# Kernel tuning notes

Hardware: AMD Instinct MI355X
Metric: run time of the kernel (lower is better)

## Reference

```python
import jax, jax.numpy as jnp
import numpy as np

N_NODES = 50000
N_EDGES = 800000
NODE_DIM = 128
HIDDEN = 256
LATENT = 128
COND = 5


def setup_inputs() -> dict:
    key = jax.random.key(0)
    ks = jax.random.split(key, 10)
    s = lambda d: 1.0 / np.sqrt(d)
    return {
        "node_features": jax.random.normal(ks[0], (N_NODES, NODE_DIM), jnp.float32),
        "conditions": jax.random.normal(ks[1], (COND,), jnp.float32),
        "src": jax.random.randint(ks[2], (N_EDGES,), 0, N_NODES, jnp.int32),
        "dst": jax.random.randint(ks[3], (N_EDGES,), 0, N_NODES, jnp.int32),
        "W1": jax.random.normal(ks[4], (NODE_DIM, HIDDEN), jnp.float32) * s(NODE_DIM),
        "b1": jnp.zeros((HIDDEN,), jnp.float32),
        "W2": jax.random.normal(ks[5], (HIDDEN, HIDDEN), jnp.float32) * s(HIDDEN),
        "b2": jnp.zeros((HIDDEN,), jnp.float32),
        "Wfc": jax.random.normal(ks[6], (HIDDEN + COND, LATENT), jnp.float32) * s(HIDDEN + COND),
        "bfc": jnp.zeros((LATENT,), jnp.float32),
        "Wmean": jax.random.normal(ks[7], (LATENT, LATENT), jnp.float32) * s(LATENT),
        "bmean": jnp.zeros((LATENT,), jnp.float32),
        "Wlogvar": jax.random.normal(ks[8], (LATENT, LATENT), jnp.float32) * s(LATENT),
        "blogvar": jnp.zeros((LATENT,), jnp.float32),
    }


def _graph_conv(x, src, dst, W, b, n_nodes):
    # gather source-node features along edges, sum-aggregate onto targets,
    # then linear transform: standard GraphConv (sum aggregation)
    agg = jax.ops.segment_sum(x[src], dst, num_segments=n_nodes)  # [N, d]
    return agg @ W + b


def reference(node_features, conditions, src, dst,
              W1, b1, W2, b2, Wfc, bfc, Wmean, bmean, Wlogvar, blogvar):
    n = node_features.shape[0]
    x = jax.nn.relu(_graph_conv(node_features, src, dst, W1, b1, n))  # [N, H]
    x = jax.nn.relu(_graph_conv(x, src, dst, W2, b2, n))              # [N, H]
    pooled = jnp.mean(x, axis=0)                                      # [H]
    h = jax.nn.relu(jnp.concatenate([pooled, conditions], axis=-1) @ Wfc + bfc)
    z_mean = h @ Wmean + bmean
    z_logvar = h @ Wlogvar + blogvar
    return z_mean, z_logvar
```

## Files before the change

kernel.cpp:

```cpp
#include <hip/hip_runtime.h>

#define N_NODES   50000
#define N_EDGES   800000
#define NODE_DIM  128
#define HIDDEN    256
#define LATENT    128
#define COND      5

#define NB        196
#define P1_CHUNK  4096
#define P1_GRID   ((N_EDGES + P1_CHUNK - 1) / P1_CHUNK)

typedef unsigned int uint;
typedef unsigned short ushort;
typedef unsigned char uchar;

typedef __attribute__((ext_vector_type(8))) short bf16x8;
typedef __attribute__((ext_vector_type(4))) float f32x4;

static __device__ __forceinline__ ushort f32_to_bf16(float f) {
    union { float f; uint u; } v; v.f = f;
    uint r = v.u + 0x7FFF + ((v.u >> 16) & 1);
    return (ushort)(r >> 16);
}
static __device__ __forceinline__ uint pack_bf16(float lo, float hi) {
    return (uint)f32_to_bf16(lo) | ((uint)f32_to_bf16(hi) << 16);
}

static __device__ __forceinline__ void gload_lds16(const void* g, void* l) {
    __builtin_amdgcn_global_load_lds(
        (const __attribute__((address_space(1))) unsigned int*)(unsigned long long)(uintptr_t)g,
        (__attribute__((address_space(3))) unsigned int*)(unsigned int)(uintptr_t)l,
        16, 0, 0);
}


#if __has_builtin(__builtin_amdgcn_cvt_pk_f32_fp8) && __has_builtin(__builtin_amdgcn_cvt_pk_fp8_f32)
#define HW_FP8 1
#endif

#ifndef HW_FP8
static __device__ __forceinline__ float dec1_fp8(uint b) {
    uint sgn = b & 0x80, mag = b & 0x7f;
    float v;
    if (mag >= 8) {
        union { uint u; float f; } t;
        t.u = (((mag >> 3) + 120) << 23) | ((mag & 7) << 20);
        v = t.f;
    } else {
        v = (float)mag * 0.001953125f;
    }
    return sgn ? -v : v;
}
static __device__ __forceinline__ uchar enc1_fp8(float f) {
    float a = fabsf(f);
    uint s = (f < 0.f) ? 0x80u : 0u;
    if (!(a >= 0.015625f)) {
        int q = (int)(a * 512.f + 0.5f);
        if (q > 7) q = 7;
        return (uchar)(s | (uint)q);
    }
    if (a >= 448.f) return (uchar)(s | 0x7E);
    union { float f; uint u; } t; t.f = a;
    uint e = (t.u >> 23) - 120;
    uint m = (t.u >> 20) & 7;
    uint rem = t.u & 0xFFFFF;
    uint v = (e << 3) | m;
    if (rem > 0x80000 || (rem == 0x80000 && (v & 1))) v++;
    if (v > 0x7E) v = 0x7E;
    return (uchar)(s | v);
}
#endif

static __device__ __forceinline__ void dec4_add(uint u, float* acc) {
#ifdef HW_FP8
    auto lo = __builtin_amdgcn_cvt_pk_f32_fp8((int)u, false);
    auto hi = __builtin_amdgcn_cvt_pk_f32_fp8((int)u, true);
    acc[0] += lo[0]; acc[1] += lo[1]; acc[2] += hi[0]; acc[3] += hi[1];
#else
    acc[0] += dec1_fp8(u & 0xff);
    acc[1] += dec1_fp8((u >> 8) & 0xff);
    acc[2] += dec1_fp8((u >> 16) & 0xff);
    acc[3] += dec1_fp8(u >> 24);
#endif
}
static __device__ __forceinline__ void dec2_add(uint u, float* acc) {
#ifdef HW_FP8
    auto lo = __builtin_amdgcn_cvt_pk_f32_fp8((int)u, false);
    acc[0] += lo[0]; acc[1] += lo[1];
#else
    acc[0] += dec1_fp8(u & 0xff);
    acc[1] += dec1_fp8((u >> 8) & 0xff);
#endif
}
static __device__ __forceinline__ uint enc2_fp8(float a, float b) {
#ifdef HW_FP8
    return (uint)__builtin_amdgcn_cvt_pk_fp8_f32(a, b, 0, false) & 0xFFFFu;
#else
    return (uint)enc1_fp8(a) | ((uint)enc1_fp8(b) << 8);
#endif
}
static __device__ __forceinline__ uchar enc1(float v) {
#ifdef HW_FP8
    return (uchar)(__builtin_amdgcn_cvt_pk_fp8_f32(v, v, 0, false) & 0xff);
#else
    return enc1_fp8(v);
#endif
}


#define NF4   (N_NODES * NODE_DIM / 4)
#define PREP1 (NF4 + NODE_DIM * HIDDEN)
#define PREP2 (PREP1 + HIDDEN * HIDDEN)
#define PREP3 (PREP2 + HIDDEN)
#define PREP4 (PREP3 + NB)
#define PREP5 (PREP4 + NB)
#define PREP6 (PREP5 + 1)

__global__ void prep_kernel(const float* __restrict__ nf,
                            const float* __restrict__ W1, const float* __restrict__ W2,
                            uchar* __restrict__ nf_fp8,
                            ushort* __restrict__ Wst1, ushort* __restrict__ Wst2,
                            float* __restrict__ pooled,
                            int* __restrict__ bcount, int* __restrict__ bcursor2,
                            int* __restrict__ hcnt) {
    int id = blockIdx.x * blockDim.x + threadIdx.x;
    if (id < NF4) {
        float4 v = reinterpret_cast<const float4*>(nf)[id];
        uint w = enc2_fp8(v.x, v.y) | (enc2_fp8(v.z, v.w) << 16);
        reinterpret_cast<uint*>(nf_fp8)[id] = w;
    } else if (id < PREP1) {
        int i = id - NF4;
        int k = i >> 8, c = i & 255;
        int idx = ((((k >> 5) * 16) + (((k & 31) >> 3) * 4 + (c >> 6))) * 64 + (c & 63)) * 8 + (k & 7);
        Wst1[idx] = f32_to_bf16(W1[i]);
    } else if (id < PREP2) {
        int i = id - PREP1;
        int k = i >> 8, c = i & 255;
        int idx = ((((k >> 5) * 16) + (((k & 31) >> 3) * 4 + (c >> 6))) * 64 + (c & 63)) * 8 + (k & 7);
        Wst2[idx] = f32_to_bf16(W2[i]);
    } else if (id < PREP3) {
        pooled[id - PREP2] = 0.f;
    } else if (id < PREP4) {
        bcount[id - PREP3] = 0;
    } else if (id < PREP5) {
        bcursor2[id - PREP4] = 0;
    } else if (id < PREP6) {
        hcnt[0] = 0;
    }
}


__global__ __launch_bounds__(256) void bcount_kernel(const int* __restrict__ dst,
                                                     int* __restrict__ bcount) {
    __shared__ int cnt[NB];
    const int t = threadIdx.x;
    for (int i = t; i < NB; i += 256) cnt[i] = 0;
    __syncthreads();
    const int base = blockIdx.x * P1_CHUNK;
#pragma unroll
    for (int i = 0; i < 16; ++i) {
        int e = base + i * 256 + t;
        if (e < N_EDGES) atomicAdd(&cnt[dst[e] >> 8], 1);
    }
    __syncthreads();
    for (int i = t; i < NB; i += 256)
        if (cnt[i] > 0) atomicAdd(&bcount[i], cnt[i]);
}

__global__ __launch_bounds__(256) void bwrite_kernel(const int* __restrict__ src,
                                                     const int* __restrict__ dst,
                                                     const int* __restrict__ bcount,
                                                     int* __restrict__ bcursor2,
                                                     uint* __restrict__ pair_buf) {
    __shared__ int s[256];
    __shared__ int cnt[NB];
    __shared__ int gbase[NB];
    const int t = threadIdx.x;
    s[t] = (t < NB) ? bcount[t] : 0;
    __syncthreads();
    for (int off = 1; off < 256; off <<= 1) {
        int v = (t >= off) ? s[t - off] : 0;
        __syncthreads();
        s[t] += v;
        __syncthreads();
    }
    for (int i = t; i < NB; i += 256) cnt[i] = 0;
    __syncthreads();

    const int base = blockIdx.x * P1_CHUNK;
    uint pk[16];
    int  bk[16], lr[16];
    bool ok[16];
#pragma unroll
    for (int i = 0; i < 16; ++i) {
        int e = base + i * 256 + t;
        ok[i] = e < N_EDGES;
        if (ok[i]) {
            int sv = src[e], d = dst[e];
            pk[i] = (uint)sv | ((uint)d << 16);
            bk[i] = d >> 8;
        }
    }
#pragma unroll
    for (int i = 0; i < 16; ++i)
        if (ok[i]) lr[i] = atomicAdd(&cnt[bk[i]], 1);
    __syncthreads();
    if (t < NB) {
        int c = cnt[t];
        if (c > 0) gbase[t] = ((t > 0) ? s[t - 1] : 0) + atomicAdd(&bcursor2[t], c);
    }
    __syncthreads();
#pragma unroll
    for (int i = 0; i < 16; ++i)
        if (ok[i]) pair_buf[gbase[bk[i]] + lr[i]] = pk[i];
}

__global__ __launch_bounds__(256) void csrloc_kernel(const uint* __restrict__ pair_buf,
                                                     const int* __restrict__ bcount,
                                                     int* __restrict__ offsets,
                                                     ushort* __restrict__ csr) {
    __shared__ int s[256];
    __shared__ int lcnt[256];
    __shared__ int loff[256];
    __shared__ int lcur[256];
    const int t = threadIdx.x;
    const int b = blockIdx.x;
    s[t] = (t < NB) ? bcount[t] : 0;
    __syncthreads();
    for (int off = 1; off < 256; off <<= 1) {
        int v = (t >= off) ? s[t - off] : 0;
        __syncthreads();
        s[t] += v;
        __syncthreads();
    }
    const int e0 = (b > 0) ? s[b - 1] : 0;
    const int e1 = s[b];
    lcnt[t] = 0;
    lcur[t] = 0;
    __syncthreads();

    for (int j = e0 + t; j < e1; j += 256)
        atomicAdd(&lcnt[(pair_buf[j] >> 16) & 255], 1);
    __syncthreads();

    const int myc = lcnt[t];
    s[t] = myc;
    __syncthreads();
    for (int off = 1; off < 256; off <<= 1) {
        int v = (t >= off) ? s[t - off] : 0;
        __syncthreads();
        s[t] += v;
        __syncthreads();
    }
    const int lofft = s[t] - myc;
    loff[t] = lofft;
    const int node = (b << 8) + t;
    if (node < N_NODES) offsets[node] = e0 + lofft;
    if (b == 0 && t == 0) offsets[N_NODES] = N_EDGES;
    __syncthreads();

    for (int j = e0 + t; j < e1; j += 256) {
        uint p = pair_buf[j];
        int dl = (int)(p >> 16) & 255;
        int r = atomicAdd(&lcur[dl], 1);
        csr[e0 + loff[dl] + r] = (ushort)(p & 0xFFFFu);
    }
}


template <int D>
__global__ __launch_bounds__(256) void agg_kernel(const uchar* __restrict__ x,
                                                  const int* __restrict__ offsets,
                                                  const ushort* __restrict__ csr,
                                                  ushort* __restrict__ out) {
    constexpr int BPL = D / 64;
    int node = (blockIdx.x * blockDim.x + threadIdx.x) >> 6;
    int lane = threadIdx.x & 63;
    if (node >= N_NODES) return;
    int j0 = __builtin_amdgcn_readfirstlane(offsets[node]);
    int j1 = __builtin_amdgcn_readfirstlane(offsets[node + 1]);

    float acc[BPL];
#pragma unroll
    for (int i = 0; i < BPL; ++i) acc[i] = 0.f;

    const uchar* base = x + lane * BPL;
    const int il = lane & 15;

    int idxv = (j0 + il < j1) ? (int)csr[j0 + il] : 0;

    for (int jb = j0; jb < j1; jb += 16) {
        int idxn = (jb + 16 + il < j1) ? (int)csr[jb + 16 + il] : 0;
        int n = j1 - jb; n = (n > 16) ? 16 : n;
        uint u[16];
        if (n == 16) {
#pragma unroll
            for (int i = 0; i < 16; ++i) {
                int s = __shfl(idxv, i);
                if constexpr (BPL == 4)
                    u[i] = *reinterpret_cast<const uint*>(base + (size_t)s * D);
                else
                    u[i] = *reinterpret_cast<const ushort*>(base + (size_t)s * D);
            }
#pragma unroll
            for (int i = 0; i < 16; ++i) {
                if constexpr (BPL == 4) dec4_add(u[i], acc); else dec2_add(u[i], acc);
            }
        } else {
#pragma unroll
            for (int i = 0; i < 16; ++i) {
                if (i < n) {
                    int s = __shfl(idxv, i);
                    if constexpr (BPL == 4)
                        u[i] = *reinterpret_cast<const uint*>(base + (size_t)s * D);
                    else
                        u[i] = *reinterpret_cast<const ushort*>(base + (size_t)s * D);
                }
            }
#pragma unroll
            for (int i = 0; i < 16; ++i) {
                if (i < n) {
                    if constexpr (BPL == 4) dec4_add(u[i], acc); else dec2_add(u[i], acc);
                }
            }
        }
        idxv = idxn;
    }

    if constexpr (BPL == 4) {
        uint2 o;
        o.x = pack_bf16(acc[0], acc[1]);
        o.y = pack_bf16(acc[2], acc[3]);
        *reinterpret_cast<uint2*>(out + (size_t)node * D + lane * 4) = o;
    } else {
        *reinterpret_cast<uint*>(out + (size_t)node * D + lane * 2) = pack_bf16(acc[0], acc[1]);
    }
}


__global__ __launch_bounds__(256) void gemm1_kernel(const ushort* __restrict__ A,
                                                    const ushort* __restrict__ Wst,
                                                    const float* __restrict__ bias,
                                                    uchar* __restrict__ Xout, int nblk) {
    constexpr int K = NODE_DIM;
    constexpr int NSTEP = K / 32;
    constexpr int WB    = NSTEP * 8 * 1024;
    constexpr int AB    = NSTEP * 4 * 1024;
    constexpr int NT    = (N_NODES + 63) / 64;
    __shared__ uchar lds[WB + 2 * AB];

    const int t    = threadIdx.x;
    const int lane = t & 63;
    const int wv   = t >> 6;
    const int fr   = lane & 15;
    const int kgl  = lane >> 4;
    const int colhalf = blockIdx.x & 1;
    const int stride  = nblk >> 1;

    const int kx = (lane & 3) ^ ((lane >> 3) & 3);

#pragma unroll
    for (int j = 0; j < NSTEP * 2; ++j) {
        const int lc = wv * (NSTEP * 2) + j;
        const int ks = lc >> 3, r = lc & 7;
        const int kg = r >> 1, ccl = r & 1;
        gload_lds16(Wst + ((size_t)ks * 16 + kg * 4 + colhalf * 2 + ccl) * 512 + lane * 8,
                    &lds[lc * 1024]);
    }

    auto stageA = [&](int buf, int row0) {
#pragma unroll
        for (int j = 0; j < NSTEP; ++j) {
            const int c  = wv * NSTEP + j;
            const int ks = c >> 2, rt = c & 3;
            gload_lds16(A + (size_t)(row0 + rt * 16 + (lane >> 2)) * K + ks * 32 + kx * 8,
                        &lds[WB + buf * AB + c * 1024]);
        }
    };

    const int rowsel = (wv & 1) * 2;
    const int colsel = wv >> 1;
    const int col0   = colhalf * 128 + colsel * 64;
    float bcol[4];
#pragma unroll
    for (int ct = 0; ct < 4; ++ct) bcol[ct] = bias[col0 + ct * 16 + fr];
    const int mrow = kgl * 4;
    const int aswz = (kgl ^ ((fr >> 1) & 3)) * 16;

    int tile = blockIdx.x >> 1;
    stageA(0, tile * 64);
    __syncthreads();

    for (int buf = 0; tile < NT; tile += stride, buf ^= 1) {
        const int tn = tile + stride;
        if (tn < NT) stageA(buf ^ 1, tn * 64);

        f32x4 acc[2][4];
#pragma unroll
        for (int rt = 0; rt < 2; ++rt)
#pragma unroll
            for (int ct = 0; ct < 4; ++ct)
                acc[rt][ct] = (f32x4){0.f, 0.f, 0.f, 0.f};

        const uchar* ab = &lds[WB + buf * AB];
#pragma unroll
        for (int ks = 0; ks < NSTEP; ++ks) {
            bf16x8 af[2], bfv[4];
#pragma unroll
            for (int rt = 0; rt < 2; ++rt)
                af[rt] = *reinterpret_cast<const bf16x8*>(ab + (ks * 4 + rowsel + rt) * 1024 + fr * 64 + aswz);
#pragma unroll
            for (int ct = 0; ct < 4; ++ct)
                bfv[ct] = *reinterpret_cast<const bf16x8*>(&lds[(ks * 8 + kgl * 2 + colsel) * 1024 + (ct * 16 + fr) * 16]);
#pragma unroll
            for (int rt = 0; rt < 2; ++rt)
#pragma unroll
                for (int ct = 0; ct < 4; ++ct)
                    acc[rt][ct] = __builtin_amdgcn_mfma_f32_16x16x32_bf16(af[rt], bfv[ct], acc[rt][ct], 0, 0, 0);
        }

        const int rowbase = tile * 64 + (wv & 1) * 32;
#pragma unroll
        for (int rt = 0; rt < 2; ++rt) {
#pragma unroll
            for (int e = 0; e < 4; ++e) {
                int m = rowbase + rt * 16 + mrow + e;
                if (m < N_NODES) {
#pragma unroll
                    for (int ct = 0; ct < 4; ++ct) {
                        float v = fmaxf(acc[rt][ct][e] + bcol[ct], 0.f);
                        Xout[(size_t)m * HIDDEN + col0 + ct * 16 + fr] = enc1(v);
                    }
                }
            }
        }
        __syncthreads();
    }
}


__global__ __launch_bounds__(256) void gemm2_kernel(const ushort* __restrict__ A,
                                                    const ushort* __restrict__ Wst,
                                                    const float* __restrict__ bias,
                                                    float* __restrict__ pooled, int nblk,
                                                    const float* __restrict__ cond,
                                                    const float* __restrict__ Wfc,
                                                    const float* __restrict__ bfc,
                                                    const float* __restrict__ Wmean,
                                                    const float* __restrict__ bmean,
                                                    const float* __restrict__ Wlogvar,
                                                    const float* __restrict__ blogvar,
                                                    float* __restrict__ outv,
                                                    int* __restrict__ hcnt) {
    constexpr int K   = HIDDEN;
    constexpr int WB  = 32768;
    constexpr int AB  = 16384;
    constexpr int NT  = (N_NODES + 31) / 32;
    __shared__ uchar lds[WB + 2 * AB];
    __shared__ int lastflag;

    const int t    = threadIdx.x;
    const int lane = t & 63;
    const int wv   = t >> 6;
    const int fr   = lane & 15;
    const int kgl  = lane >> 4;
    const int colq    = blockIdx.x & 3;
    const int stride  = nblk >> 2;

    const int kx = (lane & 3) ^ ((lane >> 3) & 3);

#pragma unroll
    for (int j = 0; j < 8; ++j) {
        const int lc = wv * 8 + j;
        const int ks = lc >> 2, kg = lc & 3;
        gload_lds16(Wst + ((size_t)ks * 16 + kg * 4 + colq) * 512 + lane * 8,
                    &lds[lc * 1024]);
    }

    auto stageA = [&](int buf, int row0) {
#pragma unroll
        for (int j = 0; j < 4; ++j) {
            const int c  = wv * 4 + j;
            const int ks = c >> 1, rh = c & 1;
            gload_lds16(A + (size_t)(row0 + rh * 16 + (lane >> 2)) * K + ks * 32 + kx * 8,
                        &lds[WB + buf * AB + c * 1024]);
        }
    };

    const int rowhalf = wv & 1;
    const int colh32  = wv >> 1;
    const int col0    = colq * 64 + colh32 * 32;
    float bcol[2];
#pragma unroll
    for (int ct = 0; ct < 2; ++ct) bcol[ct] = bias[col0 + ct * 16 + fr];
    const int mrow = kgl * 4;
    const int aswz = (kgl ^ ((fr >> 1) & 3)) * 16;

    float cs[2] = {0.f, 0.f};
    int tile = blockIdx.x >> 2;
    stageA(0, tile * 32);
    __syncthreads();

    for (int buf = 0; tile < NT; tile += stride, buf ^= 1) {
        const int tn = tile + stride;
        if (tn < NT) stageA(buf ^ 1, tn * 32);

        f32x4 acc[2];
        acc[0] = (f32x4){0.f, 0.f, 0.f, 0.f};
        acc[1] = (f32x4){0.f, 0.f, 0.f, 0.f};

        const uchar* ab = &lds[WB + buf * AB];
#pragma unroll
        for (int ks = 0; ks < 8; ++ks) {
            bf16x8 af, bfv[2];
            af = *reinterpret_cast<const bf16x8*>(ab + (ks * 2 + rowhalf) * 1024 + fr * 64 + aswz);
#pragma unroll
            for (int ct = 0; ct < 2; ++ct)
                bfv[ct] = *reinterpret_cast<const bf16x8*>(
                    &lds[(ks * 4 + kgl) * 1024 + (colh32 * 32 + ct * 16 + fr) * 16]);
#pragma unroll
            for (int ct = 0; ct < 2; ++ct)
                acc[ct] = __builtin_amdgcn_mfma_f32_16x16x32_bf16(af, bfv[ct], acc[ct], 0, 0, 0);
        }

        const int rowbase = tile * 32 + rowhalf * 16;
#pragma unroll
        for (int e = 0; e < 4; ++e) {
            int m = rowbase + mrow + e;
            if (m < N_NODES) {
                cs[0] += fmaxf(acc[0][e] + bcol[0], 0.f);
                cs[1] += fmaxf(acc[1][e] + bcol[1], 0.f);
            }
        }
        __syncthreads();
    }

#pragma unroll
    for (int ct = 0; ct < 2; ++ct) {
        cs[ct] += __shfl_xor(cs[ct], 16);
        cs[ct] += __shfl_xor(cs[ct], 32);
    }
    if (lane < 16) {
#pragma unroll
        for (int ct = 0; ct < 2; ++ct)
            atomicAdd(&pooled[col0 + ct * 16 + lane], cs[ct]);
    }

    asm volatile("s_waitcnt vmcnt(0)" ::: "memory");
    __syncthreads();
    if (t == 0) lastflag = (atomicAdd(hcnt, 1) == nblk - 1) ? 1 : 0;
    __syncthreads();
    if (lastflag) {
        float* hv = (float*)lds;
        float* hh = (float*)(lds + 2048);
        if (t < HIDDEN) hv[t] = atomicAdd(&pooled[t], 0.0f) * (1.0f / N_NODES);
        if (t < COND) hv[HIDDEN + t] = cond[t];
        __syncthreads();
        if (t < LATENT) {
            float s = bfc[t];
            for (int k = 0; k < HIDDEN + COND; ++k) s += hv[k] * Wfc[k * LATENT + t];
            hh[t] = fmaxf(s, 0.f);
        }
        __syncthreads();
        if (t < LATENT) {
            float s = bmean[t];
            for (int k = 0; k < LATENT; ++k) s += hh[k] * Wmean[k * LATENT + t];
            outv[t] = s;
        } else if (t < 2 * LATENT) {
            int j = t - LATENT;
            float s = blogvar[j];
            for (int k = 0; k < LATENT; ++k) s += hh[k] * Wlogvar[k * LATENT + j];
            outv[LATENT + j] = s;
        }
    }
}


extern "C" void kernel_launch(void* const* d_in, const int* in_sizes, int n_in,
                              void* d_out, int out_size, void* d_ws, size_t ws_size,
                              hipStream_t stream) {
    const float* node_features = (const float*)d_in[0];
    const float* conditions    = (const float*)d_in[1];
    const int*   src           = (const int*)d_in[2];
    const int*   dst           = (const int*)d_in[3];
    const float* W1  = (const float*)d_in[4];
    const float* b1  = (const float*)d_in[5];
    const float* W2  = (const float*)d_in[6];
    const float* b2  = (const float*)d_in[7];
    const float* Wfc = (const float*)d_in[8];
    const float* bfc = (const float*)d_in[9];
    const float* Wmean   = (const float*)d_in[10];
    const float* bmean   = (const float*)d_in[11];
    const float* Wlogvar = (const float*)d_in[12];
    const float* blogvar = (const float*)d_in[13];
    float* out = (float*)d_out;

    size_t o = 0;
    auto alloc = [&](size_t bytes) {
        void* p = (char*)d_ws + o;
        o += (bytes + 255) & ~(size_t)255;
        return p;
    };
    int* offsets   = (int*)alloc((size_t)(N_NODES + 1) * 4);
    int* bcount    = (int*)alloc((size_t)NB * 4);
    int* bcursor2  = (int*)alloc((size_t)NB * 4);
    int* hcnt      = (int*)alloc(4);
    uint* pair_buf = (uint*)alloc((size_t)N_EDGES * 4);
    ushort* csr    = (ushort*)alloc((size_t)N_EDGES * 2);
    float* pooled  = (float*)alloc(HIDDEN * 4);
    ushort* Wst1   = (ushort*)alloc((size_t)HIDDEN * NODE_DIM * 2);
    ushort* Wst2   = (ushort*)alloc((size_t)HIDDEN * HIDDEN * 2);
    uchar* nf_fp8  = (uchar*)alloc((size_t)N_NODES * NODE_DIM);
    uchar* x1_fp8  = (uchar*)alloc((size_t)N_NODES * HIDDEN);
    ushort* agg1   = (ushort*)alloc((size_t)(N_NODES + 64) * NODE_DIM * 2);
    ushort* agg2   = (ushort*)alloc((size_t)(N_NODES + 64) * HIDDEN * 2);

    prep_kernel<<<(PREP6 + 255) / 256, 256, 0, stream>>>(
        node_features, W1, W2, nf_fp8, Wst1, Wst2, pooled, bcount, bcursor2, hcnt);

    bcount_kernel<<<P1_GRID, 256, 0, stream>>>(dst, bcount);
    bwrite_kernel<<<P1_GRID, 256, 0, stream>>>(src, dst, bcount, bcursor2, pair_buf);
    csrloc_kernel<<<NB, 256, 0, stream>>>(pair_buf, bcount, offsets, csr);

    const int AGG_GRID = (N_NODES * 64 + 255) / 256;
    const int G1_BLK = 512;
    const int G2_BLK = 512;

    agg_kernel<NODE_DIM><<<AGG_GRID, 256, 0, stream>>>(nf_fp8, offsets, csr, agg1);
    gemm1_kernel<<<G1_BLK, 256, 0, stream>>>(agg1, Wst1, b1, x1_fp8, G1_BLK);

    agg_kernel<HIDDEN><<<AGG_GRID, 256, 0, stream>>>(x1_fp8, offsets, csr, agg2);
    gemm2_kernel<<<G2_BLK, 256, 0, stream>>>(
        agg2, Wst2, b2, pooled, G2_BLK,
        conditions, Wfc, bfc, Wmean, bmean, Wlogvar, blogvar, out, hcnt);
}
```

Baseline: 143.3 us.

## Store aggregated features as fp8 and dequantize to bf16 inside GEMM loads

New measurement: 152.2 us. +6.2%, slower.

```diff
diff --git a/kernel.cpp b/kernel.cpp
--- a/kernel.cpp
+++ b/kernel.cpp
@@ -39,7 +39,6 @@
 #define HW_FP8 1
 #endif
 
-#ifndef HW_FP8
 static __device__ __forceinline__ float dec1_fp8(uint b) {
     uint sgn = b & 0x80, mag = b & 0x7f;
     float v;
@@ -52,6 +51,7 @@
     }
     return sgn ? -v : v;
 }
+#ifndef HW_FP8
 static __device__ __forceinline__ uchar enc1_fp8(float f) {
     float a = fabsf(f);
     uint s = (f < 0.f) ? 0x80u : 0u;
@@ -106,6 +106,31 @@
 #else
     return enc1_fp8(v);
 #endif
+}
+
+static __device__ __forceinline__ bf16x8 fp8x8_to_bf16x8(uint lo, uint hi) {
+    float f[8];
+#ifdef HW_FP8
+    auto a = __builtin_amdgcn_cvt_pk_f32_fp8((int)lo, false);
+    auto b = __builtin_amdgcn_cvt_pk_f32_fp8((int)lo, true);
+    auto c = __builtin_amdgcn_cvt_pk_f32_fp8((int)hi, false);
+    auto d = __builtin_amdgcn_cvt_pk_f32_fp8((int)hi, true);
+    f[0] = a[0]; f[1] = a[1]; f[2] = b[0]; f[3] = b[1];
+    f[4] = c[0]; f[5] = c[1]; f[6] = d[0]; f[7] = d[1];
+#else
+    f[0] = dec1_fp8(lo & 0xff); f[1] = dec1_fp8((lo >> 8) & 0xff);
+    f[2] = dec1_fp8((lo >> 16) & 0xff); f[3] = dec1_fp8(lo >> 24);
+    f[4] = dec1_fp8(hi & 0xff); f[5] = dec1_fp8((hi >> 8) & 0xff);
+    f[6] = dec1_fp8((hi >> 16) & 0xff); f[7] = dec1_fp8(hi >> 24);
+#endif
+    union { uint u[4]; bf16x8 v; } r;
+    r.u[0] = pack_bf16(f[0], f[1]); r.u[1] = pack_bf16(f[2], f[3]);
+    r.u[2] = pack_bf16(f[4], f[5]); r.u[3] = pack_bf16(f[6], f[7]);
+    return r.v;
+}
+
+static __device__ __forceinline__ int swz(int slot, int r) {
+    return (slot & ~7) | ((slot ^ r) & 7);
 }
 
 
@@ -273,7 +298,7 @@
 __global__ __launch_bounds__(256) void agg_kernel(const uchar* __restrict__ x,
                                                   const int* __restrict__ offsets,
                                                   const ushort* __restrict__ csr,
-                                                  ushort* __restrict__ out) {
+                                                  uchar* __restrict__ out) {
     constexpr int BPL = D / 64;
     int node = (blockIdx.x * blockDim.x + threadIdx.x) >> 6;
     int lane = threadIdx.x & 63;
@@ -329,25 +354,22 @@
     }
 
     if constexpr (BPL == 4) {
-        uint2 o;
-        o.x = pack_bf16(acc[0], acc[1]);
-        o.y = pack_bf16(acc[2], acc[3]);
-        *reinterpret_cast<uint2*>(out + (size_t)node * D + lane * 4) = o;
+        uint o = enc2_fp8(acc[0], acc[1]) | (enc2_fp8(acc[2], acc[3]) << 16);
+        *reinterpret_cast<uint*>(out + (size_t)node * D + lane * 4) = o;
     } else {
-        *reinterpret_cast<uint*>(out + (size_t)node * D + lane * 2) = pack_bf16(acc[0], acc[1]);
-    }
-}
-
-
-__global__ __launch_bounds__(256) void gemm1_kernel(const ushort* __restrict__ A,
+        *reinterpret_cast<ushort*>(out + (size_t)node * D + lane * 2) = (ushort)enc2_fp8(acc[0], acc[1]);
+    }
+}
+
+
+__global__ __launch_bounds__(256) void gemm1_kernel(const uchar* __restrict__ A,
                                                     const ushort* __restrict__ Wst,
                                                     const float* __restrict__ bias,
                                                     uchar* __restrict__ Xout, int nblk) {
-    constexpr int K = NODE_DIM;
-    constexpr int NSTEP = K / 32;
-    constexpr int WB    = NSTEP * 8 * 1024;
-    constexpr int AB    = NSTEP * 4 * 1024;
-    constexpr int NT    = (N_NODES + 63) / 64;
+    constexpr int K  = NODE_DIM;
+    constexpr int WB = 32768;
+    constexpr int AB = 8192;
+    constexpr int NT = (N_NODES + 63) / 64;
     __shared__ uchar lds[WB + 2 * AB];
 
     const int t    = threadIdx.x;
@@ -355,40 +377,40 @@
     const int wv   = t >> 6;
     const int fr   = lane & 15;
     const int kgl  = lane >> 4;
-    const int colhalf = blockIdx.x & 1;
-    const int stride  = nblk >> 1;
-
-    const int kx = (lane & 3) ^ ((lane >> 3) & 3);
-
-#pragma unroll
-    for (int j = 0; j < NSTEP * 2; ++j) {
-        const int lc = wv * (NSTEP * 2) + j;
+    const int half    = nblk >> 1;
+    const int colhalf = blockIdx.x / half;
+    const int stride  = half;
+
+#pragma unroll
+    for (int j = 0; j < 8; ++j) {
+        const int lc = wv * 8 + j;
         const int ks = lc >> 3, r = lc & 7;
         const int kg = r >> 1, ccl = r & 1;
         gload_lds16(Wst + ((size_t)ks * 16 + kg * 4 + colhalf * 2 + ccl) * 512 + lane * 8,
                     &lds[lc * 1024]);
     }
 
+    const int lrr = lane >> 3, sl = lane & 7;
     auto stageA = [&](int buf, int row0) {
 #pragma unroll
-        for (int j = 0; j < NSTEP; ++j) {
-            const int c  = wv * NSTEP + j;
-            const int ks = c >> 2, rt = c & 3;
-            gload_lds16(A + (size_t)(row0 + rt * 16 + (lane >> 2)) * K + ks * 32 + kx * 8,
+        for (int j = 0; j < 2; ++j) {
+            const int c = wv * 2 + j;
+            const int rloc = c * 8 + lrr;
+            gload_lds16(A + (size_t)(row0 + rloc) * K + swz(sl, rloc & 7) * 16,
                         &lds[WB + buf * AB + c * 1024]);
         }
     };
 
-    const int rowsel = (wv & 1) * 2;
+    const int rowsel = (wv & 1) * 32;
     const int colsel = wv >> 1;
     const int col0   = colhalf * 128 + colsel * 64;
     float bcol[4];
 #pragma unroll
     for (int ct = 0; ct < 4; ++ct) bcol[ct] = bias[col0 + ct * 16 + fr];
     const int mrow = kgl * 4;
-    const int aswz = (kgl ^ ((fr >> 1) & 3)) * 16;
-
-    int tile = blockIdx.x >> 1;
+    const int sub  = (kgl & 1) * 8;
+
+    int tile = blockIdx.x % half;
     stageA(0, tile * 64);
     __syncthreads();
 
@@ -405,11 +427,15 @@
 
         const uchar* ab = &lds[WB + buf * AB];
 #pragma unroll
-        for (int ks = 0; ks < NSTEP; ++ks) {
+        for (int ks = 0; ks < 4; ++ks) {
+            const int g = ks * 2 + (kgl >> 1);
             bf16x8 af[2], bfv[4];
 #pragma unroll
-            for (int rt = 0; rt < 2; ++rt)
-                af[rt] = *reinterpret_cast<const bf16x8*>(ab + (ks * 4 + rowsel + rt) * 1024 + fr * 64 + aswz);
+            for (int rt = 0; rt < 2; ++rt) {
+                const int lr = rowsel + rt * 16 + fr;
+                uint2 a8 = *reinterpret_cast<const uint2*>(ab + lr * K + swz(g, fr & 7) * 16 + sub);
+                af[rt] = fp8x8_to_bf16x8(a8.x, a8.y);
+            }
 #pragma unroll
             for (int ct = 0; ct < 4; ++ct)
                 bfv[ct] = *reinterpret_cast<const bf16x8*>(&lds[(ks * 8 + kgl * 2 + colsel) * 1024 + (ct * 16 + fr) * 16]);
@@ -420,7 +446,7 @@
                     acc[rt][ct] = __builtin_amdgcn_mfma_f32_16x16x32_bf16(af[rt], bfv[ct], acc[rt][ct], 0, 0, 0);
         }
 
-        const int rowbase = tile * 64 + (wv & 1) * 32;
+        const int rowbase = tile * 64 + rowsel;
 #pragma unroll
         for (int rt = 0; rt < 2; ++rt) {
 #pragma unroll
@@ -440,7 +466,7 @@
 }
 
 
-__global__ __launch_bounds__(256) void gemm2_kernel(const ushort* __restrict__ A,
+__global__ __launch_bounds__(256) void gemm2_kernel(const uchar* __restrict__ A,
                                                     const ushort* __restrict__ Wst,
                                                     const float* __restrict__ bias,
                                                     float* __restrict__ pooled, int nblk,
@@ -453,10 +479,10 @@
                                                     const float* __restrict__ blogvar,
                                                     float* __restrict__ outv,
                                                     int* __restrict__ hcnt) {
-    constexpr int K   = HIDDEN;
-    constexpr int WB  = 32768;
-    constexpr int AB  = 16384;
-    constexpr int NT  = (N_NODES + 31) / 32;
+    constexpr int K  = HIDDEN;
+    constexpr int WB = 32768;
+    constexpr int AB = 8192;
+    constexpr int NT = (N_NODES + 31) / 32;
     __shared__ uchar lds[WB + 2 * AB];
     __shared__ int lastflag;
 
@@ -465,10 +491,9 @@
     const int wv   = t >> 6;
     const int fr   = lane & 15;
     const int kgl  = lane >> 4;
-    const int colq    = blockIdx.x & 3;
-    const int stride  = nblk >> 2;
-
-    const int kx = (lane & 3) ^ ((lane >> 3) & 3);
+    const int q      = nblk >> 2;
+    const int colq   = blockIdx.x / q;
+    const int stride = q;
 
 #pragma unroll
     for (int j = 0; j < 8; ++j) {
@@ -478,12 +503,13 @@
                     &lds[lc * 1024]);
     }
 
+    const int lrr = lane >> 4, sl = lane & 15;
     auto stageA = [&](int buf, int row0) {
 #pragma unroll
-        for (int j = 0; j < 4; ++j) {
-            const int c  = wv * 4 + j;
-            const int ks = c >> 1, rh = c & 1;
-            gload_lds16(A + (size_t)(row0 + rh * 16 + (lane >> 2)) * K + ks * 32 + kx * 8,
+        for (int j = 0; j < 2; ++j) {
+            const int c = wv * 2 + j;
+            const int rloc = c * 4 + lrr;
+            gload_lds16(A + (size_t)(row0 + rloc) * K + swz(sl, rloc & 7) * 16,
                         &lds[WB + buf * AB + c * 1024]);
         }
     };
@@ -495,10 +521,10 @@
 #pragma unroll
     for (int ct = 0; ct < 2; ++ct) bcol[ct] = bias[col0 + ct * 16 + fr];
     const int mrow = kgl * 4;
-    const int aswz = (kgl ^ ((fr >> 1) & 3)) * 16;
+    const int sub  = (kgl & 1) * 8;
 
     float cs[2] = {0.f, 0.f};
-    int tile = blockIdx.x >> 2;
+    int tile = blockIdx.x % q;
     stageA(0, tile * 32);
     __syncthreads();
 
@@ -511,10 +537,13 @@
         acc[1] = (f32x4){0.f, 0.f, 0.f, 0.f};
 
         const uchar* ab = &lds[WB + buf * AB];
+        const int lr = rowhalf * 16 + fr;
 #pragma unroll
         for (int ks = 0; ks < 8; ++ks) {
-            bf16x8 af, bfv[2];
-            af = *reinterpret_cast<const bf16x8*>(ab + (ks * 2 + rowhalf) * 1024 + fr * 64 + aswz);
+            const int g = ks * 2 + (kgl >> 1);
+            uint2 a8 = *reinterpret_cast<const uint2*>(ab + lr * K + swz(g, fr & 7) * 16 + sub);
+            bf16x8 af = fp8x8_to_bf16x8(a8.x, a8.y);
+            bf16x8 bfv[2];
 #pragma unroll
             for (int ct = 0; ct < 2; ++ct)
                 bfv[ct] = *reinterpret_cast<const bf16x8*>(
@@ -613,8 +642,8 @@
     ushort* Wst2   = (ushort*)alloc((size_t)HIDDEN * HIDDEN * 2);
     uchar* nf_fp8  = (uchar*)alloc((size_t)N_NODES * NODE_DIM);
     uchar* x1_fp8  = (uchar*)alloc((size_t)N_NODES * HIDDEN);
-    ushort* agg1   = (ushort*)alloc((size_t)(N_NODES + 64) * NODE_DIM * 2);
-    ushort* agg2   = (ushort*)alloc((size_t)(N_NODES + 64) * HIDDEN * 2);
+    uchar* agg1    = (uchar*)alloc((size_t)(N_NODES + 64) * NODE_DIM);
+    uchar* agg2    = (uchar*)alloc((size_t)(N_NODES + 64) * HIDDEN);
 
     prep_kernel<<<(PREP6 + 255) / 256, 256, 0, stream>>>(
         node_features, W1, W2, nf_fp8, Wst1, Wst2, pooled, bcount, bcursor2, hcnt);
@@ -624,8 +653,8 @@
     csrloc_kernel<<<NB, 256, 0, stream>>>(pair_buf, bcount, offsets, csr);
 
     const int AGG_GRID = (N_NODES * 64 + 255) / 256;
-    const int G1_BLK = 512;
-    const int G2_BLK = 512;
+    const int G1_BLK = 768;
+    const int G2_BLK = 768;
 
     agg_kernel<NODE_DIM><<<AGG_GRID, 256, 0, stream>>>(nf_fp8, offsets, csr, agg1);
     gemm1_kernel<<<G1_BLK, 256, 0, stream>>>(agg1, Wst1, b1, x1_fp8, G1_BLK);
```
